# Optimization experiments

Hardware: AMD Instinct MI355X
Metric: run time of the kernel (lower is better)

The kernel has to match this reference:

```python
import jax, jax.numpy as jnp
import numpy as np

N_ENT = 250002   # user_num + comp_num + 2
D = 128          # emb_dim
R = 12           # rel_num
T = 16           # number of timesteps (latest_train_time + 1)
E = 300000       # edges active per timestep
S = 256          # seed users per timestep
USER_NUM = 200000
COMP_NUM = 50000
T_WIN = 5        # T_ snapshot attention window in seq_GCRNN_batch
NEG = jnp.float32(-1e9)


def setup_inputs() -> dict:
    key = jax.random.key(0)
    ks = jax.random.split(key, 8)
    ent_emb = jax.random.normal(ks[0], (N_ENT, D), jnp.float32) * 0.05
    query_emb = jax.random.normal(ks[1], (N_ENT, D), jnp.float32) * 0.05
    rel_emb = jax.random.normal(ks[2], (R, D), jnp.float32) * 0.05
    edges_src = jax.random.randint(ks[3], (T, E), 0, N_ENT, jnp.int32)
    edges_dst = jax.random.randint(ks[4], (T, E), 0, N_ENT, jnp.int32)
    edges_rel = jax.random.randint(ks[5], (T, E), 0, R, jnp.int32)
    seeds = jax.random.randint(ks[6], (T, S), 0, USER_NUM, jnp.int32)
    comp_idx = jax.random.randint(ks[7], (T, S), 0, COMP_NUM, jnp.int32)
    return {
        "ent_emb": ent_emb,
        "query_emb": query_emb,
        "rel_emb": rel_emb,
        "edges_src": edges_src,
        "edges_dst": edges_dst,
        "edges_rel": edges_rel,
        "seeds": seeds,
        "comp_idx": comp_idx,
        "user_id_max": 199999,
        "comp_num": 50000,
    }


def _gcrnn(ent_emb, query_emb, rel_emb, edges_src, edges_dst, edges_rel, seeds):
    """seq_GCRNN_batch: per-step message passing + residual update + 5-snapshot attention.
    Returns seed embeddings [T, S, D] in (timestep, seed) order."""
    N = ent_emb.shape[0]

    def step(carry, xs):
        node_emb, buf, t = carry   # node_emb: [N,D], buf: [T_WIN,N,D] (rolling snapshots)
        src, dst, rel, sd = xs
        # msg_GCN: src embedding * relation embedding, gathered per edge
        msg = node_emb[src] * rel_emb[rel]                       # [E, D]
        sums = jax.ops.segment_sum(msg, dst, num_segments=N)     # [N, D]
        cnt = jax.ops.segment_sum(jnp.ones(src.shape, node_emb.dtype), dst, num_segments=N)
        # reduce_GCN: mailbox mean; update_node: residual add (only nodes that received msgs)
        mean = sums / jnp.maximum(cnt, 1.0)[:, None]
        node_emb = node_emb + jnp.where((cnt > 0)[:, None], mean, 0.0)
        # rolling window of last T_WIN snapshots
        buf = jnp.concatenate([buf[1:], node_emb[None]], axis=0)  # [T_WIN, N, D]
        # attention over snapshots for seed users (learnable_query)
        stack = buf[:, sd]                                        # [T_WIN, S, D]
        q = query_emb[sd]                                         # [S, D]
        att = jnp.einsum('tsd,sd->ts', stack, q)                  # [T_WIN, S]
        # only min(t+1, T_WIN) snapshots exist so far -> mask the rest
        valid = jnp.arange(T_WIN) >= jnp.maximum(T_WIN - 1 - t, 0)
        att = jnp.where(valid[:, None], att, NEG)
        w = jax.nn.softmax(att, axis=0)
        seed_emb = jnp.einsum('ts,tsd->sd', w, stack)             # [S, D]
        return (node_emb, buf, t + 1), seed_emb

    buf0 = jnp.zeros((T_WIN,) + ent_emb.shape, ent_emb.dtype)
    (_, _, _), seed_embs = jax.lax.scan(
        step, (ent_emb, buf0, jnp.int32(0)), (edges_src, edges_dst, edges_rel, seeds))
    return seed_embs  # [T, S, D]


def reference(ent_emb, query_emb, rel_emb, edges_src, edges_dst, edges_rel,
              seeds, comp_idx, user_id_max, comp_num):
    u = _gcrnn(ent_emb, query_emb, rel_emb, edges_src, edges_dst, edges_rel, seeds)  # [T,S,D]
    # company embeddings live at ids user_id_max+1 .. user_id_max+comp_num
    tgt = ent_emb[user_id_max + 1 + comp_idx]                     # [T, S, D]
    all_c = jax.lax.dynamic_slice_in_dim(ent_emb, user_id_max + 1, comp_num, axis=0)  # [C, D]
    pos = jnp.sum(u * tgt, axis=-1)                               # [T, S]
    scores = jnp.einsum('tsd,cd->tsc', u, all_c)                  # [T, S, C]
    loss = -jnp.sum(pos - jax.nn.logsumexp(scores, axis=-1))
    return loss
```

## Files before the change

### kernel.cpp

```cpp
#include <hip/hip_runtime.h>

#define N_ENT   250002
#define DD      128
#define T_STEPS 16
#define E_EDGES 300000
#define S_SEEDS 256
#define C_NUM   50000
#define BASE    200000
#define NB      245
#define N_PAD   (NB * 1024)
#define NBKT    245
#define BSH     10
#define CAPB    1536
#define EPB     2048
#define NGRID16 ((N_ENT + 15) / 16)
#define SEED16  (5 * S_SEEDS / 16)
#define NCG     3125
#define SCHUNK  49

typedef __attribute__((ext_vector_type(8))) short short8;
typedef __attribute__((ext_vector_type(4))) float f32x4;

__device__ inline unsigned short f2bf(float f) {
    unsigned u = __float_as_uint(f);
    u += 0x7FFFu + ((u >> 16) & 1u);
    return (unsigned short)(u >> 16);
}
__device__ inline float bf_lo(unsigned p) { return __uint_as_float(p << 16); }
__device__ inline float bf_hi(unsigned p) { return __uint_as_float(p & 0xffff0000u); }
__device__ inline unsigned pk2(float x, float y) {
    return (unsigned)f2bf(x) | ((unsigned)f2bf(y) << 16);
}

#define NODE_W (N_ENT * 64)
#define GC_W   (T_STEPS * NBKT)
__global__ __launch_bounds__(256) void init_kernel(
    const float2* __restrict__ ent2, unsigned* __restrict__ node_bf,
    int* __restrict__ gcount, float* __restrict__ rowsum, float* __restrict__ out)
{
    int gid = blockIdx.x * 256 + threadIdx.x;
    if (gid < NODE_W) {
        float2 v = ent2[gid];
        node_bf[gid] = pk2(v.x, v.y);
    } else if (gid < NODE_W + GC_W) {
        gcount[gid - NODE_W] = 0;
    } else if (gid < NODE_W + GC_W + T_STEPS * S_SEEDS) {
        rowsum[gid - NODE_W - GC_W] = 0.f;
    } else if (gid == NODE_W + GC_W + T_STEPS * S_SEEDS) {
        out[0] = 0.f;
    }
}

__global__ __launch_bounds__(256) void conv_kernel(
    const float4* __restrict__ c4, ushort4* __restrict__ cb4)
{
    int gid = blockIdx.x * 256 + threadIdx.x;
    float4 v = c4[gid];
    cb4[gid] = make_ushort4(f2bf(v.x), f2bf(v.y), f2bf(v.z), f2bf(v.w));
}

__global__ __launch_bounds__(256) void bucketA(
    const int* __restrict__ esrc, const int* __restrict__ edst, const int* __restrict__ erel,
    int* __restrict__ gcount, unsigned* __restrict__ bkt)
{
    int t = blockIdx.y;
    int base = blockIdx.x * EPB;
    int tid = threadIdx.x;
    __shared__ int lcnt[NBKT];
    __shared__ int lbase[NBKT];
    for (int i = tid; i < NBKT; i += 256) lcnt[i] = 0;
    __syncthreads();
    int dl[8], sr[8], off[8], bk[8];
    #pragma unroll
    for (int i = 0; i < 8; ++i) {
        int e = base + i * 256 + tid;
        bk[i] = -1;
        if (e < E_EDGES) {
            int eb = t * E_EDGES + e;
            int dd = edst[eb];
            sr[i] = esrc[eb] | (erel[eb] << 18);
            dl[i] = dd & ((1 << BSH) - 1);
            bk[i] = dd >> BSH;
            off[i] = atomicAdd(&lcnt[bk[i]], 1);
        }
    }
    __syncthreads();
    for (int i = tid; i < NBKT; i += 256)
        lbase[i] = atomicAdd(&gcount[t * NBKT + i], lcnt[i]);
    __syncthreads();
    #pragma unroll
    for (int i = 0; i < 8; ++i) {
        if (bk[i] >= 0) {
            int pos = lbase[bk[i]] + off[i];
            if (pos < CAPB)
                bkt[((size_t)(t * NBKT + bk[i])) * CAPB + pos] =
                    (unsigned)sr[i] | ((unsigned)dl[i] << 22);
        }
    }
}

__global__ __launch_bounds__(256) void histB(
    const int* __restrict__ gcount, const unsigned* __restrict__ bkt,
    int* __restrict__ offs, int* __restrict__ partials)
{
    int b = blockIdx.x, t = blockIdx.y, tid = threadIdx.x;
    __shared__ int cnt[1024];
    for (int i = tid; i < 1024; i += 256) cnt[i] = 0;
    __syncthreads();
    int n = min(gcount[t * NBKT + b], CAPB);
    const unsigned* bp = bkt + ((size_t)(t * NBKT + b)) * CAPB;
    for (int i = tid; i < n; i += 256)
        atomicAdd(&cnt[bp[i] >> 22], 1);
    __syncthreads();
    int* op = offs + (size_t)t * N_PAD + (b << BSH);
    for (int i = tid; i < 1024; i += 256) op[i] = cnt[i];
    if (tid == 0) partials[t * NB + b] = n;
}

__global__ __launch_bounds__(256) void scanB_kernel(int* __restrict__ partials)
{
    __shared__ int sc[256];
    int t = blockIdx.x, tid = threadIdx.x;
    int v = (tid < NB) ? partials[t * NB + tid] : 0;
    sc[tid] = v;
    __syncthreads();
    for (int off = 1; off < 256; off <<= 1) {
        int y = (tid >= off) ? sc[tid - off] : 0;
        __syncthreads();
        sc[tid] += y;
        __syncthreads();
    }
    if (tid < NB) partials[t * NB + tid] = (tid > 0) ? sc[tid - 1] : 0;
}

__global__ __launch_bounds__(256) void scanC_kernel(
    int* __restrict__ offs, const int* __restrict__ partials)
{
    int t = blockIdx.y, b = blockIdx.x, tid = threadIdx.x;
    int* base = offs + (size_t)t * N_PAD + b * 1024 + tid * 4;
    int4 v = *(const int4*)base;
    int s = v.x + v.y + v.z + v.w;
    int lane = tid & 63, wv = tid >> 6;
    int x = s;
    #pragma unroll
    for (int off = 1; off < 64; off <<= 1) {
        int y = __shfl_up(x, off, 64);
        if (lane >= off) x += y;
    }
    __shared__ int wsum[4];
    if (lane == 63) wsum[wv] = x;
    __syncthreads();
    int prefix = partials[t * NB + b];
    for (int w = 0; w < 4; ++w) prefix += (w < wv) ? wsum[w] : 0;
    int excl = prefix + x - s;
    int4 o;
    o.x = excl; o.y = o.x + v.x; o.z = o.y + v.y; o.w = o.z + v.z;
    *(int4*)base = o;
}

__global__ __launch_bounds__(256) void scatB(
    const int* __restrict__ gcount, const unsigned* __restrict__ bkt,
    const int* __restrict__ offs, unsigned* __restrict__ sortedp)
{
    int b = blockIdx.x, t = blockIdx.y, tid = threadIdx.x;
    __shared__ int cur[1024];
    const int* op = offs + (size_t)t * N_PAD + (b << BSH);
    for (int i = tid; i < 1024; i += 256) cur[i] = op[i];
    __syncthreads();
    int n = min(gcount[t * NBKT + b], CAPB);
    const unsigned* bp = bkt + ((size_t)(t * NBKT + b)) * CAPB;
    unsigned* sp = sortedp + (size_t)t * E_EDGES;
    for (int i = tid; i < n; i += 256) {
        unsigned e = bp[i];
        int pos = atomicAdd(&cur[e >> 22], 1);
        sp[pos] = e & 0x3FFFFFu;
    }
}

__global__ __launch_bounds__(256) void gather_fused(
    const unsigned* __restrict__ node_old, unsigned* __restrict__ node_new,
    const float2* __restrict__ rel2, const int* __restrict__ offs,
    const unsigned* __restrict__ sortedp, const int* __restrict__ seeds,
    float2* __restrict__ gath2, int t)
{
    int wv = threadIdx.x >> 6;
    int lane = threadIdx.x & 63;
    int grp = lane >> 4;
    int l16 = lane & 15;
    int bx = blockIdx.x;
    int n = 0, gslot = -1;
    bool active;
    if (bx < NGRID16) {
        n = bx * 16 + wv * 4 + grp;
        active = (n < N_ENT);
    } else {
        int g = (bx - NGRID16) * 16 + wv * 4 + grp;
        int j = g >> 8;
        active = (t + j < T_STEPS);
        if (active) {
            n = seeds[t * S_SEEDS + g];
            gslot = (((t + j) * 5 + (4 - j)) * S_SEEDS + (g & 255)) * 64 + l16 * 4;
        }
    }
    if (active) {
        const int* op = offs + (size_t)t * N_PAD;
        int start = op[n];
        int end = op[n + 1];
        uint4 nb = *((const uint4*)(node_old + (size_t)n * 64) + l16);
        float vx0 = bf_lo(nb.x), vy0 = bf_hi(nb.x);
        float vx1 = bf_lo(nb.y), vy1 = bf_hi(nb.y);
        float vx2 = bf_lo(nb.z), vy2 = bf_hi(nb.z);
        float vx3 = bf_lo(nb.w), vy3 = bf_hi(nb.w);
        if (end > start) {
            const unsigned* sp = sortedp + (size_t)t * E_EDGES;
            float ax0=0.f,ay0=0.f,ax1=0.f,ay1=0.f,ax2=0.f,ay2=0.f,ax3=0.f,ay3=0.f;
            for (int p = start; p < end; ++p) {
                unsigned pr = sp[p];
                uint4 sb = *((const uint4*)(node_old + (size_t)(pr & 0x3FFFFu) * 64) + l16);
                const float* rp = (const float*)(rel2 + (pr >> 18) * 64) + l16 * 8;
                float4 r01 = *(const float4*)rp;
                float4 r23 = *(const float4*)(rp + 4);
                ax0 += bf_lo(sb.x) * r01.x; ay0 += bf_hi(sb.x) * r01.y;
                ax1 += bf_lo(sb.y) * r01.z; ay1 += bf_hi(sb.y) * r01.w;
                ax2 += bf_lo(sb.z) * r23.x; ay2 += bf_hi(sb.z) * r23.y;
                ax3 += bf_lo(sb.w) * r23.z; ay3 += bf_hi(sb.w) * r23.w;
            }
            float inv = 1.0f / (float)(end - start);
            vx0 += ax0 * inv; vy0 += ay0 * inv;
            vx1 += ax1 * inv; vy1 += ay1 * inv;
            vx2 += ax2 * inv; vy2 += ay2 * inv;
            vx3 += ax3 * inv; vy3 += ay3 * inv;
        }
        uint4 o;
        o.x = pk2(vx0, vy0); o.y = pk2(vx1, vy1);
        o.z = pk2(vx2, vy2); o.w = pk2(vx3, vy3);
        if (gslot >= 0) {
            gath2[gslot + 0] = make_float2(bf_lo(o.x), bf_hi(o.x));
            gath2[gslot + 1] = make_float2(bf_lo(o.y), bf_hi(o.y));
            gath2[gslot + 2] = make_float2(bf_lo(o.z), bf_hi(o.z));
            gath2[gslot + 3] = make_float2(bf_lo(o.w), bf_hi(o.w));
        } else {
            *((uint4*)(node_new + (size_t)n * 64) + l16) = o;
        }
    }
}

__global__ __launch_bounds__(64) void attn_kernel(
    const float2* __restrict__ q2, const float2* __restrict__ g2,
    const int* __restrict__ seeds, float2* __restrict__ u2, unsigned* __restrict__ ubf)
{
    int b = blockIdx.x;
    int t = b >> 8;
    int s = b & 255;
    int lane = threadIdx.x;
    int seed = seeds[t * S_SEEDS + s];
    float2 q = q2[seed * 64 + lane];
    float2 g[5];
    float att[5];
    #pragma unroll
    for (int w = 0; w < 5; ++w) {
        float2 gv = g2[((t * 5 + w) * S_SEEDS + s) * 64 + lane];
        g[w] = gv;
        float p = gv.x * q.x + gv.y * q.y;
        #pragma unroll
        for (int off = 32; off > 0; off >>= 1) p += __shfl_xor(p, off, 64);
        att[w] = (w >= 4 - t) ? p : -1e9f;
    }
    float m = -1e30f;
    #pragma unroll
    for (int w = 0; w < 5; ++w) m = fmaxf(m, att[w]);
    float den = 0.f;
    #pragma unroll
    for (int w = 0; w < 5; ++w) den += __expf(att[w] - m);
    float invd = 1.0f / den;
    float2 o = make_float2(0.f, 0.f);
    #pragma unroll
    for (int w = 0; w < 5; ++w) {
        float wt = __expf(att[w] - m) * invd;
        o.x += wt * g[w].x;
        o.y += wt * g[w].y;
    }
    int idx = (t * S_SEEDS + s) * 64 + lane;
    u2[idx] = o;
    ubf[idx] = pk2(o.x, o.y);
}

__global__ __launch_bounds__(256) void score_mfma(
    const unsigned short* __restrict__ ub, const unsigned short* __restrict__ cb,
    float* __restrict__ rowsum)
{
    int tid = threadIdx.x;
    int wv = tid >> 6, lane = tid & 63;
    int col16 = lane & 15, quad = lane >> 4;
    int b = blockIdx.x;
    int xcd = b & 7, k = b >> 3;
    int ychunk = xcd + 8 * (k >> 4);
    int xblk = k & 15;
    int rbase = xblk * 256 + wv * 64;

    short8 B[4][4];
    #pragma unroll
    for (int s = 0; s < 4; ++s) {
        const unsigned short* bp = ub + (size_t)(rbase + s * 16 + col16) * DD + quad * 8;
        #pragma unroll
        for (int kk = 0; kk < 4; ++kk) B[s][kk] = *(const short8*)(bp + kk * 32);
    }

    float acc0 = 0.f, acc1 = 0.f, acc2 = 0.f, acc3 = 0.f;
    int c0 = ychunk * SCHUNK;
    int c1 = min(c0 + SCHUNK, NCG);
    const unsigned short* abase = cb + col16 * DD + quad * 8;

#define SCORE_STEP(AF)  do {                                                              \
        f32x4 d0 = {0.f,0.f,0.f,0.f}, d1 = {0.f,0.f,0.f,0.f};                             \
        f32x4 d2 = {0.f,0.f,0.f,0.f}, d3 = {0.f,0.f,0.f,0.f};                             \
        _Pragma("unroll")                                                                 \
        for (int kk = 0; kk < 4; ++kk) {                                                  \
            d0 = __builtin_amdgcn_mfma_f32_16x16x32_bf16(AF[kk], B[0][kk], d0, 0, 0, 0);  \
            d1 = __builtin_amdgcn_mfma_f32_16x16x32_bf16(AF[kk], B[1][kk], d1, 0, 0, 0);  \
            d2 = __builtin_amdgcn_mfma_f32_16x16x32_bf16(AF[kk], B[2][kk], d2, 0, 0, 0);  \
            d3 = __builtin_amdgcn_mfma_f32_16x16x32_bf16(AF[kk], B[3][kk], d3, 0, 0, 0);  \
        }                                                                                 \
        _Pragma("unroll")                                                                 \
        for (int r = 0; r < 4; ++r) {                                                     \
            acc0 += __expf(d0[r]); acc1 += __expf(d1[r]);                                 \
            acc2 += __expf(d2[r]); acc3 += __expf(d3[r]);                                 \
        } } while (0)

    short8 A0[4], A1[4];
    #pragma unroll
    for (int kk = 0; kk < 4; ++kk)
        A0[kk] = *(const short8*)(abase + (size_t)c0 * 2048 + kk * 32);
    int c = c0;
    for (; c + 2 <= c1; c += 2) {
        #pragma unroll
        for (int kk = 0; kk < 4; ++kk)
            A1[kk] = *(const short8*)(abase + (size_t)(c + 1) * 2048 + kk * 32);
        SCORE_STEP(A0);
        if (c + 2 < c1) {
            #pragma unroll
            for (int kk = 0; kk < 4; ++kk)
                A0[kk] = *(const short8*)(abase + (size_t)(c + 2) * 2048 + kk * 32);
        }
        SCORE_STEP(A1);
    }
    if (c < c1) SCORE_STEP(A0);

    acc0 += __shfl_xor(acc0, 16, 64); acc0 += __shfl_xor(acc0, 32, 64);
    acc1 += __shfl_xor(acc1, 16, 64); acc1 += __shfl_xor(acc1, 32, 64);
    acc2 += __shfl_xor(acc2, 16, 64); acc2 += __shfl_xor(acc2, 32, 64);
    acc3 += __shfl_xor(acc3, 16, 64); acc3 += __shfl_xor(acc3, 32, 64);
    if (quad == 0) {
        atomicAdd(&rowsum[rbase +  0 + col16], acc0);
        atomicAdd(&rowsum[rbase + 16 + col16], acc1);
        atomicAdd(&rowsum[rbase + 32 + col16], acc2);
        atomicAdd(&rowsum[rbase + 48 + col16], acc3);
    }
}

__global__ __launch_bounds__(256) void final_kernel(
    const float2* __restrict__ u2, const float* __restrict__ ent,
    const int* __restrict__ cidx, const float* __restrict__ rowsum,
    float* __restrict__ out)
{
    int wv = threadIdx.x >> 6, lane = threadIdx.x & 63;
    int row = blockIdx.x * 4 + wv;
    int ci = cidx[row];
    const float2* tp = (const float2*)(ent + (size_t)(BASE + ci) * DD);
    float2 a = u2[row * 64 + lane];
    float2 t = tp[lane];
    float p = a.x * t.x + a.y * t.y;
    #pragma unroll
    for (int off = 32; off > 0; off >>= 1) p += __shfl_xor(p, off, 64);
    if (lane == 0) atomicAdd(out, logf(rowsum[row]) - p);
}

extern "C" void kernel_launch(void* const* d_in, const int* in_sizes, int n_in,
                              void* d_out, int out_size, void* d_ws, size_t ws_size,
                              hipStream_t stream)
{
    (void)in_sizes; (void)n_in; (void)out_size; (void)ws_size;
    const float* ent   = (const float*)d_in[0];
    const float* query = (const float*)d_in[1];
    const float* rel   = (const float*)d_in[2];
    const int* esrc    = (const int*)d_in[3];
    const int* edst    = (const int*)d_in[4];
    const int* erel    = (const int*)d_in[5];
    const int* seeds   = (const int*)d_in[6];
    const int* cidx    = (const int*)d_in[7];
    float* out = (float*)d_out;

    char* ws = (char*)d_ws;
    size_t off = 0;
    unsigned* nodeA   = (unsigned*)(ws + off);       off += (size_t)N_ENT * DD * 2;
    unsigned* nodeB   = (unsigned*)(ws + off);       off += (size_t)N_ENT * DD * 2;
    int*      offs    = (int*)(ws + off);            off += (size_t)T_STEPS * N_PAD * 4;
    int*      partials= (int*)(ws + off);            off += (size_t)T_STEPS * NB * 4;
    int*      gcount  = (int*)(ws + off);            off += (size_t)T_STEPS * NBKT * 4;
    unsigned* bkt     = (unsigned*)(ws + off);       off += (size_t)T_STEPS * NBKT * CAPB * 4;
    unsigned* sortedp = (unsigned*)(ws + off);       off += (size_t)T_STEPS * E_EDGES * 4;
    float*    gath    = (float*)(ws + off);          off += (size_t)T_STEPS * 5 * S_SEEDS * DD * 4;
    float*    u       = (float*)(ws + off);          off += (size_t)T_STEPS * S_SEEDS * DD * 4;
    unsigned* ubf     = (unsigned*)(ws + off);       off += (size_t)T_STEPS * S_SEEDS * DD * 2;
    unsigned short* cb = (unsigned short*)(ws + off); off += (size_t)C_NUM * DD * 2;
    float*    rsum    = (float*)(ws + off);          off += (size_t)T_STEPS * S_SEEDS * 4;

    int init_items = NODE_W + GC_W + T_STEPS * S_SEEDS + 1;
    init_kernel<<<(init_items + 255) / 256, 256, 0, stream>>>(
        (const float2*)ent, nodeA, gcount, rsum, out);
    conv_kernel<<<C_NUM * DD / 4 / 256, 256, 0, stream>>>(
        (const float4*)(ent + (size_t)BASE * DD), (ushort4*)cb);

    dim3 bgrid((E_EDGES + EPB - 1) / EPB, T_STEPS);
    dim3 kgrid(NBKT, T_STEPS);
    bucketA<<<bgrid, 256, 0, stream>>>(esrc, edst, erel, gcount, bkt);
    histB<<<kgrid, 256, 0, stream>>>(gcount, bkt, offs, partials);
    scanB_kernel<<<T_STEPS, 256, 0, stream>>>(partials);
    scanC_kernel<<<kgrid, 256, 0, stream>>>(offs, partials);
    scatB<<<kgrid, 256, 0, stream>>>(gcount, bkt, offs, sortedp);

    unsigned* cur = nodeA;
    unsigned* nxt = nodeB;
    for (int t = 0; t < T_STEPS; ++t) {
        gather_fused<<<NGRID16 + SEED16, 256, 0, stream>>>(
            cur, nxt, (const float2*)rel, offs, sortedp, seeds, (float2*)gath, t);
        unsigned* tmp = cur; cur = nxt; nxt = tmp;
    }
    attn_kernel<<<T_STEPS * S_SEEDS, 64, 0, stream>>>(
        (const float2*)query, (const float2*)gath, seeds, (float2*)u, (unsigned*)ubf);
    score_mfma<<<1024, 256, 0, stream>>>((const unsigned short*)ubf, cb, rsum);
    final_kernel<<<T_STEPS * S_SEEDS / 4, 256, 0, stream>>>(
        (const float2*)u, ent, cidx, rsum, out);
}
```

Baseline: 1.106 ms.

## Track per-node buffer parity to skip copying untouched nodes each step

Before, every gather step rewrote all 250k node rows from the old ping-pong buffer to the new one, even for nodes that received no messages. A per-timestep parity bit for each node is now precomputed and stored in the offsets' high bit and in the sorted edge entries, so idle nodes return early and readers pick the right buffer from the parity. Separately, the exponent in the score kernel uses exp2f on company embeddings prescaled by log2(e), and the score grid is doubled with a smaller chunk size. This adds a preprocessing pass and per-edge buffer selection, and bf16 rounding of the prescaled embeddings may shift results slightly.

```diff
diff --git a/kernel.cpp b/kernel.cpp
--- a/kernel.cpp
+++ b/kernel.cpp
@@ -16,7 +16,9 @@
 #define NGRID16 ((N_ENT + 15) / 16)
 #define SEED16  (5 * S_SEEDS / 16)
 #define NCG     3125
-#define SCHUNK  49
+#define SCHUNK  25
+#define OMSK    0x7FFFFFFF
+#define LOG2E   1.44269504088896340736f
 
 typedef __attribute__((ext_vector_type(8))) short short8;
 typedef __attribute__((ext_vector_type(4))) float f32x4;
@@ -56,7 +58,8 @@
 {
     int gid = blockIdx.x * 256 + threadIdx.x;
     float4 v = c4[gid];
-    cb4[gid] = make_ushort4(f2bf(v.x), f2bf(v.y), f2bf(v.z), f2bf(v.w));
+    cb4[gid] = make_ushort4(f2bf(v.x * LOG2E), f2bf(v.y * LOG2E),
+                            f2bf(v.z * LOG2E), f2bf(v.w * LOG2E));
 }
 
 __global__ __launch_bounds__(256) void bucketA(
@@ -117,6 +120,19 @@
     if (tid == 0) partials[t * NB + b] = n;
 }
 
+__global__ __launch_bounds__(256) void vb_build(
+    const int* __restrict__ offs, unsigned char* __restrict__ vbarr)
+{
+    int n = blockIdx.x * 256 + threadIdx.x;
+    if (n >= N_ENT) return;
+    int v = 0;
+    #pragma unroll
+    for (int t = 0; t < T_STEPS; ++t) {
+        vbarr[(size_t)t * N_PAD + n] = (unsigned char)v;
+        v ^= (offs[(size_t)t * N_PAD + n] > 0) ? 1 : 0;
+    }
+}
+
 __global__ __launch_bounds__(256) void scanB_kernel(int* __restrict__ partials)
 {
     __shared__ int sc[256];
@@ -134,7 +150,8 @@
 }
 
 __global__ __launch_bounds__(256) void scanC_kernel(
-    int* __restrict__ offs, const int* __restrict__ partials)
+    int* __restrict__ offs, const int* __restrict__ partials,
+    const unsigned char* __restrict__ vbarr)
 {
     int t = blockIdx.y, b = blockIdx.x, tid = threadIdx.x;
     int* base = offs + (size_t)t * N_PAD + b * 1024 + tid * 4;
@@ -155,30 +172,38 @@
     int excl = prefix + x - s;
     int4 o;
     o.x = excl; o.y = o.x + v.x; o.z = o.y + v.y; o.w = o.z + v.z;
+    uchar4 vb4 = *(const uchar4*)(vbarr + (size_t)t * N_PAD + b * 1024 + tid * 4);
+    o.x |= ((int)vb4.x) << 31;
+    o.y |= ((int)vb4.y) << 31;
+    o.z |= ((int)vb4.z) << 31;
+    o.w |= ((int)vb4.w) << 31;
     *(int4*)base = o;
 }
 
 __global__ __launch_bounds__(256) void scatB(
     const int* __restrict__ gcount, const unsigned* __restrict__ bkt,
-    const int* __restrict__ offs, unsigned* __restrict__ sortedp)
+    const int* __restrict__ offs, const unsigned char* __restrict__ vbarr,
+    unsigned* __restrict__ sortedp)
 {
     int b = blockIdx.x, t = blockIdx.y, tid = threadIdx.x;
     __shared__ int cur[1024];
     const int* op = offs + (size_t)t * N_PAD + (b << BSH);
-    for (int i = tid; i < 1024; i += 256) cur[i] = op[i];
+    for (int i = tid; i < 1024; i += 256) cur[i] = op[i] & OMSK;
     __syncthreads();
     int n = min(gcount[t * NBKT + b], CAPB);
     const unsigned* bp = bkt + ((size_t)(t * NBKT + b)) * CAPB;
     unsigned* sp = sortedp + (size_t)t * E_EDGES;
+    const unsigned char* vbt = vbarr + (size_t)t * N_PAD;
     for (int i = tid; i < n; i += 256) {
         unsigned e = bp[i];
         int pos = atomicAdd(&cur[e >> 22], 1);
-        sp[pos] = e & 0x3FFFFFu;
+        unsigned src = e & 0x3FFFFu;
+        sp[pos] = (e & 0x3FFFFFu) | ((unsigned)vbt[src] << 22);
     }
 }
 
 __global__ __launch_bounds__(256) void gather_fused(
-    const unsigned* __restrict__ node_old, unsigned* __restrict__ node_new,
+    const unsigned* __restrict__ node0, unsigned* __restrict__ node1,
     const float2* __restrict__ rel2, const int* __restrict__ offs,
     const unsigned* __restrict__ sortedp, const int* __restrict__ seeds,
     float2* __restrict__ gath2, int t)
@@ -204,9 +229,14 @@
     }
     if (active) {
         const int* op = offs + (size_t)t * N_PAD;
-        int start = op[n];
-        int end = op[n + 1];
-        uint4 nb = *((const uint4*)(node_old + (size_t)n * 64) + l16);
+        int sraw = op[n];
+        int eraw = op[n + 1];
+        int start = sraw & OMSK;
+        int end = eraw & OMSK;
+        if (end == start && gslot < 0) return;
+        unsigned vb = (unsigned)sraw >> 31;
+        const unsigned* selfb = vb ? node1 : node0;
+        uint4 nb = *((const uint4*)(selfb + (size_t)n * 64) + l16);
         float vx0 = bf_lo(nb.x), vy0 = bf_hi(nb.x);
         float vx1 = bf_lo(nb.y), vy1 = bf_hi(nb.y);
         float vx2 = bf_lo(nb.z), vy2 = bf_hi(nb.z);
@@ -216,8 +246,9 @@
             float ax0=0.f,ay0=0.f,ax1=0.f,ay1=0.f,ax2=0.f,ay2=0.f,ax3=0.f,ay3=0.f;
             for (int p = start; p < end; ++p) {
                 unsigned pr = sp[p];
-                uint4 sb = *((const uint4*)(node_old + (size_t)(pr & 0x3FFFFu) * 64) + l16);
-                const float* rp = (const float*)(rel2 + (pr >> 18) * 64) + l16 * 8;
+                const unsigned* gb = (pr & (1u << 22)) ? node1 : node0;
+                uint4 sb = *((const uint4*)(gb + (size_t)(pr & 0x3FFFFu) * 64) + l16);
+                const float* rp = (const float*)(rel2 + ((pr >> 18) & 15u) * 64) + l16 * 8;
                 float4 r01 = *(const float4*)rp;
                 float4 r23 = *(const float4*)(rp + 4);
                 ax0 += bf_lo(sb.x) * r01.x; ay0 += bf_hi(sb.x) * r01.y;
@@ -240,7 +271,8 @@
             gath2[gslot + 2] = make_float2(bf_lo(o.z), bf_hi(o.z));
             gath2[gslot + 3] = make_float2(bf_lo(o.w), bf_hi(o.w));
         } else {
-            *((uint4*)(node_new + (size_t)n * 64) + l16) = o;
+            unsigned* outb = vb ? (unsigned*)node0 : node1;
+            *((uint4*)(outb + (size_t)n * 64) + l16) = o;
         }
     }
 }
@@ -323,38 +355,40 @@
         }                                                                                 \
         _Pragma("unroll")                                                                 \
         for (int r = 0; r < 4; ++r) {                                                     \
-            acc0 += __expf(d0[r]); acc1 += __expf(d1[r]);                                 \
-            acc2 += __expf(d2[r]); acc3 += __expf(d3[r]);                                 \
+            acc0 += exp2f(d0[r]); acc1 += exp2f(d1[r]);                                   \
+            acc2 += exp2f(d2[r]); acc3 += exp2f(d3[r]);                                   \
         } } while (0)
 
-    short8 A0[4], A1[4];
-    #pragma unroll
-    for (int kk = 0; kk < 4; ++kk)
-        A0[kk] = *(const short8*)(abase + (size_t)c0 * 2048 + kk * 32);
-    int c = c0;
-    for (; c + 2 <= c1; c += 2) {
+    if (c0 < c1) {
+        short8 A0[4], A1[4];
         #pragma unroll
         for (int kk = 0; kk < 4; ++kk)
-            A1[kk] = *(const short8*)(abase + (size_t)(c + 1) * 2048 + kk * 32);
-        SCORE_STEP(A0);
-        if (c + 2 < c1) {
+            A0[kk] = *(const short8*)(abase + (size_t)c0 * 2048 + kk * 32);
+        int c = c0;
+        for (; c + 2 <= c1; c += 2) {
             #pragma unroll
             for (int kk = 0; kk < 4; ++kk)
-                A0[kk] = *(const short8*)(abase + (size_t)(c + 2) * 2048 + kk * 32);
-        }
-        SCORE_STEP(A1);
-    }
-    if (c < c1) SCORE_STEP(A0);
-
-    acc0 += __shfl_xor(acc0, 16, 64); acc0 += __shfl_xor(acc0, 32, 64);
-    acc1 += __shfl_xor(acc1, 16, 64); acc1 += __shfl_xor(acc1, 32, 64);
-    acc2 += __shfl_xor(acc2, 16, 64); acc2 += __shfl_xor(acc2, 32, 64);
-    acc3 += __shfl_xor(acc3, 16, 64); acc3 += __shfl_xor(acc3, 32, 64);
-    if (quad == 0) {
-        atomicAdd(&rowsum[rbase +  0 + col16], acc0);
-        atomicAdd(&rowsum[rbase + 16 + col16], acc1);
-        atomicAdd(&rowsum[rbase + 32 + col16], acc2);
-        atomicAdd(&rowsum[rbase + 48 + col16], acc3);
+                A1[kk] = *(const short8*)(abase + (size_t)(c + 1) * 2048 + kk * 32);
+            SCORE_STEP(A0);
+            if (c + 2 < c1) {
+                #pragma unroll
+                for (int kk = 0; kk < 4; ++kk)
+                    A0[kk] = *(const short8*)(abase + (size_t)(c + 2) * 2048 + kk * 32);
+            }
+            SCORE_STEP(A1);
+        }
+        if (c < c1) SCORE_STEP(A0);
+
+        acc0 += __shfl_xor(acc0, 16, 64); acc0 += __shfl_xor(acc0, 32, 64);
+        acc1 += __shfl_xor(acc1, 16, 64); acc1 += __shfl_xor(acc1, 32, 64);
+        acc2 += __shfl_xor(acc2, 16, 64); acc2 += __shfl_xor(acc2, 32, 64);
+        acc3 += __shfl_xor(acc3, 16, 64); acc3 += __shfl_xor(acc3, 32, 64);
+        if (quad == 0) {
+            atomicAdd(&rowsum[rbase +  0 + col16], acc0);
+            atomicAdd(&rowsum[rbase + 16 + col16], acc1);
+            atomicAdd(&rowsum[rbase + 32 + col16], acc2);
+            atomicAdd(&rowsum[rbase + 48 + col16], acc3);
+        }
     }
 }
 
@@ -392,13 +426,14 @@
 
     char* ws = (char*)d_ws;
     size_t off = 0;
-    unsigned* nodeA   = (unsigned*)(ws + off);       off += (size_t)N_ENT * DD * 2;
-    unsigned* nodeB   = (unsigned*)(ws + off);       off += (size_t)N_ENT * DD * 2;
+    unsigned* node0   = (unsigned*)(ws + off);       off += (size_t)N_ENT * DD * 2;
+    unsigned* node1   = (unsigned*)(ws + off);       off += (size_t)N_ENT * DD * 2;
     int*      offs    = (int*)(ws + off);            off += (size_t)T_STEPS * N_PAD * 4;
     int*      partials= (int*)(ws + off);            off += (size_t)T_STEPS * NB * 4;
     int*      gcount  = (int*)(ws + off);            off += (size_t)T_STEPS * NBKT * 4;
     unsigned* bkt     = (unsigned*)(ws + off);       off += (size_t)T_STEPS * NBKT * CAPB * 4;
     unsigned* sortedp = (unsigned*)(ws + off);       off += (size_t)T_STEPS * E_EDGES * 4;
+    unsigned char* vbarr = (unsigned char*)(ws + off); off += (size_t)T_STEPS * N_PAD;
     float*    gath    = (float*)(ws + off);          off += (size_t)T_STEPS * 5 * S_SEEDS * DD * 4;
     float*    u       = (float*)(ws + off);          off += (size_t)T_STEPS * S_SEEDS * DD * 4;
     unsigned* ubf     = (unsigned*)(ws + off);       off += (size_t)T_STEPS * S_SEEDS * DD * 2;
@@ -407,7 +442,7 @@
 
     int init_items = NODE_W + GC_W + T_STEPS * S_SEEDS + 1;
     init_kernel<<<(init_items + 255) / 256, 256, 0, stream>>>(
-        (const float2*)ent, nodeA, gcount, rsum, out);
+        (const float2*)ent, node0, gcount, rsum, out);
     conv_kernel<<<C_NUM * DD / 4 / 256, 256, 0, stream>>>(
         (const float4*)(ent + (size_t)BASE * DD), (ushort4*)cb);
 
@@ -415,20 +450,18 @@
     dim3 kgrid(NBKT, T_STEPS);
     bucketA<<<bgrid, 256, 0, stream>>>(esrc, edst, erel, gcount, bkt);
     histB<<<kgrid, 256, 0, stream>>>(gcount, bkt, offs, partials);
+    vb_build<<<(N_ENT + 255) / 256, 256, 0, stream>>>(offs, vbarr);
     scanB_kernel<<<T_STEPS, 256, 0, stream>>>(partials);
-    scanC_kernel<<<kgrid, 256, 0, stream>>>(offs, partials);
-    scatB<<<kgrid, 256, 0, stream>>>(gcount, bkt, offs, sortedp);
-
-    unsigned* cur = nodeA;
-    unsigned* nxt = nodeB;
+    scanC_kernel<<<kgrid, 256, 0, stream>>>(offs, partials, vbarr);
+    scatB<<<kgrid, 256, 0, stream>>>(gcount, bkt, offs, vbarr, sortedp);
+
     for (int t = 0; t < T_STEPS; ++t) {
         gather_fused<<<NGRID16 + SEED16, 256, 0, stream>>>(
-            cur, nxt, (const float2*)rel, offs, sortedp, seeds, (float2*)gath, t);
-        unsigned* tmp = cur; cur = nxt; nxt = tmp;
+            node0, node1, (const float2*)rel, offs, sortedp, seeds, (float2*)gath, t);
     }
     attn_kernel<<<T_STEPS * S_SEEDS, 64, 0, stream>>>(
         (const float2*)query, (const float2*)gath, seeds, (float2*)u, (unsigned*)ubf);
-    score_mfma<<<1024, 256, 0, stream>>>((const unsigned short*)ubf, cb, rsum);
+    score_mfma<<<2048, 256, 0, stream>>>((const unsigned short*)ubf, cb, rsum);
     final_kernel<<<T_STEPS * S_SEEDS / 4, 256, 0, stream>>>(
         (const float2*)u, ent, cidx, rsum, out);
 }
```

New measurement: 1.106 ms. Within noise of the previous version (-0.0%).
